# Performance work log

Hardware: AMD Instinct MI355X
Metric: run time of the kernel (lower is better)

The kernel has to match this reference:

```python
import jax, jax.numpy as jnp
import numpy as np

B, KD, VD = 65536, 512, 512

def setup_inputs() -> dict:
    key = jax.random.key(0)
    ks = jax.random.split(key, 5)
    return {
        "k": jax.random.normal(ks[0], (B, KD), jnp.float32),
        "v": jax.random.normal(ks[1], (B, VD), jnp.float32),
        "W": jax.random.normal(ks[2], (VD, KD), jnp.float32) * 0.02,  # memory.weight
        "S": jax.random.normal(ks[3], (VD, KD), jnp.float32) * 0.01,  # momentum buffer
        "gate_w": jax.random.normal(ks[4], (3, KD), jnp.float32) * 0.02,
        "gate_b": jnp.full((3,), 0.5, jnp.float32),  # nn.init.constant_(bias, 0.5)
    }

def reference(k, v, W, S, gate_w, gate_b):
    sg = jax.lax.stop_gradient
    # memory lookup: Linear(key_dim -> val_dim), no bias
    retrieved = k @ W.T                           # (B, VD)
    diff = retrieved - sg(v)
    loss_memory = jnp.mean(diff * diff)
    # --- TTT update (training path; all detached from autodiff in torch) ---
    # autograd.grad of mse(memory(k), v) w.r.t. W is analytically an outer product:
    # grad = 2/(B*VD) * (k @ W.T - v).T @ k
    d = sg(diff)                                  # loss_ttt uses detached k, v -> same residual values
    grad = (2.0 / (B * VD)) * (d.T @ sg(k))       # (VD, KD)
    # gates from batch-mean key
    gates = jax.nn.sigmoid(gate_w @ sg(jnp.mean(k, axis=0)) + gate_b)  # (3,)
    alpha, eta, theta = gates[0], gates[1], gates[2]
    new_S = eta * sg(S) - theta * grad            # momentum decay + gradient step
    new_W = (1.0 - alpha) * sg(W) + new_S         # gated weight decay + momentum write
    return retrieved, loss_memory, new_W, new_S
```

## Files before the change

kernel.cpp:

```cpp
#include <hip/hip_runtime.h>
#include <hip/hip_bf16.h>

typedef __attribute__((ext_vector_type(8))) short bf16x8;
typedef __attribute__((ext_vector_type(4))) float f32x4;
typedef unsigned int u32;
typedef unsigned short u16;

#define NB 65536
#define NKD 512
#define NVD 512

#define WS_COLSUM 262144
#define WS_LOSS   262656
#define WS_DIFFT_BYTES 1056768

#define OUT_LOSS 33554432
#define OUT_W    33554433
#define OUT_S    33816577

__device__ inline u32 pkbf2(float a, float b) {
    __hip_bfloat162 h2 = __float22bfloat162_rn(make_float2(a, b));
    u32 r;
    __builtin_memcpy(&r, &h2, 4);
    return r;
}

__device__ inline void async16(const u16* g, u16* l) {
    __builtin_amdgcn_global_load_lds(
        (const __attribute__((address_space(1))) u32*)g,
        (__attribute__((address_space(3))) u32*)l, 16, 0, 0);
}

#define PA 72
#define PT 136

__global__ __launch_bounds__(256, 2)
void k1_gemm1(const float* __restrict__ kmat, const float* __restrict__ vmat,
              const float* __restrict__ Wmat, float* __restrict__ out,
              float* __restrict__ ws, u16* __restrict__ diffT) {
    __shared__ u16 sm[18432];
    __shared__ float lred[4];

    const int tid = threadIdx.x;
    const int bx = blockIdx.x;
    const int rowtile = bx >> 2, ntile = bx & 3;
    const long b0 = (long)rowtile * 128;
    const int vd0 = ntile * 128;
    const int wv = tid >> 6, lane = tid & 63;
    const int wm = wv & 1, wn = wv >> 1;
    const int col = lane & 15, kg = lane >> 4;

    const int srow = tid >> 4;
    const int scol = (tid & 15) * 4;

    f32x4 acc[4][4] = {};

    for (int it = 0; it < 8; ++it) {
        __syncthreads();
        const float* gA = kmat + (b0 + srow) * 512 + it * 64 + scol;
        const float* gB = Wmat + (long)(vd0 + srow) * 512 + it * 64 + scol;
#pragma unroll
        for (int i = 0; i < 8; ++i) {
            float4 a = *(const float4*)(gA + (long)i * 16 * 512);
            float4 b = *(const float4*)(gB + (long)i * 16 * 512);
            int r = i * 16 + srow;
            *(uint2*)&sm[r * PA + scol] = make_uint2(pkbf2(a.x, a.y), pkbf2(a.z, a.w));
            *(uint2*)&sm[9216 + r * PA + scol] = make_uint2(pkbf2(b.x, b.y), pkbf2(b.z, b.w));
        }
        __syncthreads();
#pragma unroll
        for (int kk = 0; kk < 2; ++kk) {
            bf16x8 af[4], bfr[4];
#pragma unroll
            for (int i = 0; i < 4; ++i)
                af[i] = *(const bf16x8*)&sm[(wm * 64 + i * 16 + col) * PA + kk * 32 + kg * 8];
#pragma unroll
            for (int j = 0; j < 4; ++j)
                bfr[j] = *(const bf16x8*)&sm[9216 + (wn * 64 + j * 16 + col) * PA + kk * 32 + kg * 8];
#pragma unroll
            for (int i = 0; i < 4; ++i)
#pragma unroll
                for (int j = 0; j < 4; ++j)
                    acc[i][j] = __builtin_amdgcn_mfma_f32_16x16x32_bf16(af[i], bfr[j], acc[i][j], 0, 0, 0);
        }
    }

    __syncthreads();
    u16* smT = sm;

    float lossp = 0.f;
    const int rg = lane >> 4;
#pragma unroll
    for (int i = 0; i < 4; ++i) {
#pragma unroll
        for (int j = 0; j < 4; ++j) {
            int r0 = wm * 64 + i * 16 + rg * 4;
            int c  = wn * 64 + j * 16 + col;
            long gb = b0 + r0;
            float dd[4];
#pragma unroll
            for (int r = 0; r < 4; ++r) {
                float rv = acc[i][j][r];
                long gidx = (gb + r) * 512 + vd0 + c;
                out[gidx] = rv;
                float dv = rv - vmat[gidx];
                lossp += dv * dv;
                dd[r] = dv;
            }
            *(u32*)&smT[c * PT + r0]     = pkbf2(dd[0], dd[1]);
            *(u32*)&smT[c * PT + r0 + 2] = pkbf2(dd[2], dd[3]);
        }
    }

#pragma unroll
    for (int m = 32; m; m >>= 1) lossp += __shfl_xor(lossp, m);
    if (lane == 0) lred[wv] = lossp;
    __syncthreads();
    if (tid == 0) atomicAdd(&ws[WS_LOSS], lred[0] + lred[1] + lred[2] + lred[3]);

    {
        const int c = tid >> 1, h = tid & 1;
        const u16* src = &smT[c * PT + h * 64];
        u16* dst = diffT + ((long)(vd0 + c) << 16) + b0 + h * 64;
#pragma unroll
        for (int q = 0; q < 8; ++q) {
            uint4 t4 = *(const uint4*)(src + q * 8);
            *(uint4*)(dst + q * 8) = t4;
        }
    }
}

__global__ __launch_bounds__(256, 2)
void k2_grad(const u16* __restrict__ diffT, const float* __restrict__ kmat,
             float* __restrict__ ws) {
    __shared__ u16 sm[17408];
    u16* As = sm;
    u16* Bs = sm + 8192;

    const int tid = threadIdx.x;
    const int bx = blockIdx.x;
    const int tile = bx & 15, chunk = bx >> 4;
    const int vd0 = (tile >> 2) * 128, kd0 = (tile & 3) * 128;
    const long b0 = (long)chunk * 2048;
    const int wv = tid >> 6, lane = tid & 63;
    const int wm = wv & 1, wn = wv >> 1;
    const int col = lane & 15, kg = lane >> 4;

    const int bcol = (tid & 63) * 2;
    const int bq = wv * 16;

    f32x4 acc[4][4] = {};
    float cs0 = 0.f, cs1 = 0.f;

    for (int it = 0; it < 32; ++it) {
        __syncthreads();
        {
            const u16* gbase = diffT + ((long)vd0 << 16) + b0 + it * 64;
#pragma unroll
            for (int q = 0; q < 4; ++q) {
                int rowb = wv * 32 + q * 8;
                const u16* g = gbase + ((long)(rowb + (lane >> 3)) << 16) + (lane & 7) * 8;
                async16(g, &As[rowb * 64]);
            }
        }
        {
            const float* gk = kmat + (b0 + it * 64 + bq) * 512 + kd0 + bcol;
            float2 r[16];
#pragma unroll
            for (int i = 0; i < 16; ++i) r[i] = *(const float2*)(gk + (long)i * 512);
#pragma unroll
            for (int i = 0; i < 16; ++i) { cs0 += r[i].x; cs1 += r[i].y; }
            u32 p0[8], p1[8];
#pragma unroll
            for (int i = 0; i < 8; ++i) {
                p0[i] = pkbf2(r[2 * i].x, r[2 * i + 1].x);
                p1[i] = pkbf2(r[2 * i].y, r[2 * i + 1].y);
            }
            *(uint4*)&Bs[bcol * PA + bq]           = make_uint4(p0[0], p0[1], p0[2], p0[3]);
            *(uint4*)&Bs[bcol * PA + bq + 8]       = make_uint4(p0[4], p0[5], p0[6], p0[7]);
            *(uint4*)&Bs[(bcol + 1) * PA + bq]     = make_uint4(p1[0], p1[1], p1[2], p1[3]);
            *(uint4*)&Bs[(bcol + 1) * PA + bq + 8] = make_uint4(p1[4], p1[5], p1[6], p1[7]);
        }
        __syncthreads();
#pragma unroll
        for (int kk = 0; kk < 2; ++kk) {
            bf16x8 af[4], bfr[4];
#pragma unroll
            for (int i = 0; i < 4; ++i)
                af[i] = *(const bf16x8*)&As[(wm * 64 + i * 16 + col) * 64 + kk * 32 + kg * 8];
#pragma unroll
            for (int j = 0; j < 4; ++j)
                bfr[j] = *(const bf16x8*)&Bs[(wn * 64 + j * 16 + col) * PA + kk * 32 + kg * 8];
#pragma unroll
            for (int i = 0; i < 4; ++i)
#pragma unroll
                for (int j = 0; j < 4; ++j)
                    acc[i][j] = __builtin_amdgcn_mfma_f32_16x16x32_bf16(af[i], bfr[j], acc[i][j], 0, 0, 0);
        }
    }

    const int rg = lane >> 4;
#pragma unroll
    for (int i = 0; i < 4; ++i)
#pragma unroll
        for (int j = 0; j < 4; ++j)
#pragma unroll
            for (int r = 0; r < 4; ++r) {
                int vd = vd0 + wm * 64 + i * 16 + rg * 4 + r;
                int kd = kd0 + wn * 64 + j * 16 + col;
                atomicAdd(&ws[vd * 512 + kd], acc[i][j][r]);
            }

    if (vd0 == 0) {
        __syncthreads();
        float* cred = (float*)sm;
        cred[bcol * 4 + wv] = cs0;
        cred[(bcol + 1) * 4 + wv] = cs1;
        __syncthreads();
        if (tid < 128) {
            float s = cred[tid * 4] + cred[tid * 4 + 1] + cred[tid * 4 + 2] + cred[tid * 4 + 3];
            atomicAdd(&ws[WS_COLSUM + kd0 + tid], s);
        }
    }
}

__global__ __launch_bounds__(256)
void k3_final(const float* __restrict__ Wmat, const float* __restrict__ Smat,
              const float* __restrict__ gw, const float* __restrict__ gb,
              const float* __restrict__ ws, float* __restrict__ out) {
    __shared__ float gates[3];
    const int tid = threadIdx.x;
    if (tid < 64) {
        float d0 = 0.f, d1 = 0.f, d2 = 0.f;
#pragma unroll
        for (int i = 0; i < 8; ++i) {
            int kd = i * 64 + tid;
            float km = ws[WS_COLSUM + kd] * (1.0f / 65536.0f);
            d0 += gw[kd] * km;
            d1 += gw[512 + kd] * km;
            d2 += gw[1024 + kd] * km;
        }
#pragma unroll
        for (int m = 32; m; m >>= 1) {
            d0 += __shfl_xor(d0, m);
            d1 += __shfl_xor(d1, m);
            d2 += __shfl_xor(d2, m);
        }
        if (tid == 0) {
            gates[0] = 1.f / (1.f + __expf(-(d0 + gb[0])));
            gates[1] = 1.f / (1.f + __expf(-(d1 + gb[1])));
            gates[2] = 1.f / (1.f + __expf(-(d2 + gb[2])));
        }
    }
    __syncthreads();
    const float alpha = gates[0], eta = gates[1], theta = gates[2];
    const int i = blockIdx.x * 256 + tid;
    float g = ws[i] * 5.9604644775390625e-8f;
    float ns = eta * Smat[i] - theta * g;
    out[OUT_S + i] = ns;
    out[OUT_W + i] = (1.f - alpha) * Wmat[i] + ns;
    if (blockIdx.x == 0 && tid == 0)
        out[OUT_LOSS] = ws[WS_LOSS] * 2.98023223876953125e-8f;
}

extern "C" void kernel_launch(void* const* d_in, const int* in_sizes, int n_in,
                              void* d_out, int out_size, void* d_ws, size_t ws_size,
                              hipStream_t stream) {
    const float* k  = (const float*)d_in[0];
    const float* v  = (const float*)d_in[1];
    const float* W  = (const float*)d_in[2];
    const float* S  = (const float*)d_in[3];
    const float* gw = (const float*)d_in[4];
    const float* gb = (const float*)d_in[5];
    float* out = (float*)d_out;
    float* ws  = (float*)d_ws;
    u16* diffT = (u16*)((char*)d_ws + WS_DIFFT_BYTES);

    hipMemsetAsync(d_ws, 0, (WS_LOSS + 1) * sizeof(float), stream);

    hipLaunchKernelGGL(k1_gemm1, dim3(2048), dim3(256), 0, stream, k, v, W, out, ws, diffT);
    hipLaunchKernelGGL(k2_grad,  dim3(512),  dim3(256), 0, stream, diffT, k, ws);
    hipLaunchKernelGGL(k3_final, dim3(1024), dim3(256), 0, stream, W, S, gw, gb, ws, out);
}
```

Before: 566.8 us.

## Replace residual-based gradient with Gram-matrix formulation and trace-based loss

```diff
diff --git a/kernel.cpp b/kernel.cpp
--- a/kernel.cpp
+++ b/kernel.cpp
@@ -6,13 +6,14 @@
 typedef unsigned int u32;
 typedef unsigned short u16;
 
-#define NB 65536
-#define NKD 512
-#define NVD 512
-
-#define WS_COLSUM 262144
-#define WS_LOSS   262656
-#define WS_DIFFT_BYTES 1056768
+#define WS_G1     0
+#define WS_G2     262144
+#define WS_COLSUM 524288
+#define WS_VSQ    524800
+#define WS_GATES  524801
+#define WS_TR1    524804
+#define WS_TR2    524805
+#define WS_PART   524808
 
 #define OUT_LOSS 33554432
 #define OUT_W    33554433
@@ -25,177 +26,199 @@
     return r;
 }
 
-__device__ inline void async16(const u16* g, u16* l) {
-    __builtin_amdgcn_global_load_lds(
-        (const __attribute__((address_space(1))) u32*)g,
-        (__attribute__((address_space(3))) u32*)l, 16, 0, 0);
-}
-
-#define PA 72
-#define PT 136
-
-__global__ __launch_bounds__(256, 2)
-void k1_gemm1(const float* __restrict__ kmat, const float* __restrict__ vmat,
-              const float* __restrict__ Wmat, float* __restrict__ out,
-              float* __restrict__ ws, u16* __restrict__ diffT) {
+__device__ inline void jobdec(int j, int& isG2, int& rt, int& ct) {
+    if (j >= 10) { isG2 = 1; rt = (j - 10) >> 2; ct = (j - 10) & 3; }
+    else {
+        isG2 = 0;
+        if (j < 4)      { rt = 0; ct = j; }
+        else if (j < 7) { rt = 1; ct = j - 3; }
+        else if (j < 9) { rt = 2; ct = j - 5; }
+        else            { rt = 3; ct = 3; }
+    }
+}
+
+__global__ __launch_bounds__(256, 3)
+void kg_gram(const float* __restrict__ kmat, const float* __restrict__ vmat,
+             float* __restrict__ ws) {
     __shared__ u16 sm[18432];
-    __shared__ float lred[4];
+    u16* As = sm;
+    u16* Bs = sm + 9216;
 
     const int tid = threadIdx.x;
     const int bx = blockIdx.x;
-    const int rowtile = bx >> 2, ntile = bx & 3;
-    const long b0 = (long)rowtile * 128;
-    const int vd0 = ntile * 128;
+    const int c = bx & 31;
+    const int j = bx >> 5;
+    int isG2, rt, ct;
+    jobdec(j, isG2, rt, ct);
+    const float* Asrc = (isG2 ? vmat : kmat) + rt * 128;
+    const float* Bsrc = kmat + ct * 128;
+    const bool doCS = isG2 && (rt == 0);
+    const bool doVS = isG2 && (ct == 0);
+    const long b0 = (long)c * 2048;
+
     const int wv = tid >> 6, lane = tid & 63;
     const int wm = wv & 1, wn = wv >> 1;
     const int col = lane & 15, kg = lane >> 4;
-
-    const int srow = tid >> 4;
-    const int scol = (tid & 15) * 4;
+    const int bcol = (tid & 63) * 2;
+    const int bq = wv * 16;
 
     f32x4 acc[4][4] = {};
-
-    for (int it = 0; it < 8; ++it) {
-        __syncthreads();
-        const float* gA = kmat + (b0 + srow) * 512 + it * 64 + scol;
-        const float* gB = Wmat + (long)(vd0 + srow) * 512 + it * 64 + scol;
-#pragma unroll
-        for (int i = 0; i < 8; ++i) {
-            float4 a = *(const float4*)(gA + (long)i * 16 * 512);
-            float4 b = *(const float4*)(gB + (long)i * 16 * 512);
-            int r = i * 16 + srow;
-            *(uint2*)&sm[r * PA + scol] = make_uint2(pkbf2(a.x, a.y), pkbf2(a.z, a.w));
-            *(uint2*)&sm[9216 + r * PA + scol] = make_uint2(pkbf2(b.x, b.y), pkbf2(b.z, b.w));
-        }
-        __syncthreads();
+    float cs0 = 0.f, cs1 = 0.f, vs = 0.f;
+
+    float2 aR[16], bR[16];
+    {
+        const float* ga = Asrc + (b0 + bq) * 512 + bcol;
+        const float* gb = Bsrc + (b0 + bq) * 512 + bcol;
+#pragma unroll
+        for (int i = 0; i < 16; ++i) {
+            aR[i] = *(const float2*)(ga + (long)i * 512);
+            bR[i] = *(const float2*)(gb + (long)i * 512);
+        }
+    }
+
+    for (int it = 0; it < 32; ++it) {
+        __syncthreads();
+        if (doVS) {
+#pragma unroll
+            for (int i = 0; i < 16; ++i) vs += aR[i].x * aR[i].x + aR[i].y * aR[i].y;
+        }
+        if (doCS) {
+#pragma unroll
+            for (int i = 0; i < 16; ++i) { cs0 += bR[i].x; cs1 += bR[i].y; }
+        }
+        *(uint4*)&As[bcol * 72 + bq] = make_uint4(
+            pkbf2(aR[0].x, aR[1].x), pkbf2(aR[2].x, aR[3].x),
+            pkbf2(aR[4].x, aR[5].x), pkbf2(aR[6].x, aR[7].x));
+        *(uint4*)&As[bcol * 72 + bq + 8] = make_uint4(
+            pkbf2(aR[8].x, aR[9].x), pkbf2(aR[10].x, aR[11].x),
+            pkbf2(aR[12].x, aR[13].x), pkbf2(aR[14].x, aR[15].x));
+        *(uint4*)&As[(bcol + 1) * 72 + bq] = make_uint4(
+            pkbf2(aR[0].y, aR[1].y), pkbf2(aR[2].y, aR[3].y),
+            pkbf2(aR[4].y, aR[5].y), pkbf2(aR[6].y, aR[7].y));
+        *(uint4*)&As[(bcol + 1) * 72 + bq + 8] = make_uint4(
+            pkbf2(aR[8].y, aR[9].y), pkbf2(aR[10].y, aR[11].y),
+            pkbf2(aR[12].y, aR[13].y), pkbf2(aR[14].y, aR[15].y));
+        *(uint4*)&Bs[bcol * 72 + bq] = make_uint4(
+            pkbf2(bR[0].x, bR[1].x), pkbf2(bR[2].x, bR[3].x),
+            pkbf2(bR[4].x, bR[5].x), pkbf2(bR[6].x, bR[7].x));
+        *(uint4*)&Bs[bcol * 72 + bq + 8] = make_uint4(
+            pkbf2(bR[8].x, bR[9].x), pkbf2(bR[10].x, bR[11].x),
+            pkbf2(bR[12].x, bR[13].x), pkbf2(bR[14].x, bR[15].x));
+        *(uint4*)&Bs[(bcol + 1) * 72 + bq] = make_uint4(
+            pkbf2(bR[0].y, bR[1].y), pkbf2(bR[2].y, bR[3].y),
+            pkbf2(bR[4].y, bR[5].y), pkbf2(bR[6].y, bR[7].y));
+        *(uint4*)&Bs[(bcol + 1) * 72 + bq + 8] = make_uint4(
+            pkbf2(bR[8].y, bR[9].y), pkbf2(bR[10].y, bR[11].y),
+            pkbf2(bR[12].y, bR[13].y), pkbf2(bR[14].y, bR[15].y));
+        __syncthreads();
+        if (it < 31) {
+            const float* ga = Asrc + (b0 + (it + 1) * 64 + bq) * 512 + bcol;
+            const float* gb = Bsrc + (b0 + (it + 1) * 64 + bq) * 512 + bcol;
+#pragma unroll
+            for (int i = 0; i < 16; ++i) {
+                aR[i] = *(const float2*)(ga + (long)i * 512);
+                bR[i] = *(const float2*)(gb + (long)i * 512);
+            }
+        }
 #pragma unroll
         for (int kk = 0; kk < 2; ++kk) {
             bf16x8 af[4], bfr[4];
 #pragma unroll
             for (int i = 0; i < 4; ++i)
-                af[i] = *(const bf16x8*)&sm[(wm * 64 + i * 16 + col) * PA + kk * 32 + kg * 8];
-#pragma unroll
-            for (int j = 0; j < 4; ++j)
-                bfr[j] = *(const bf16x8*)&sm[9216 + (wn * 64 + j * 16 + col) * PA + kk * 32 + kg * 8];
+                af[i] = *(const bf16x8*)&As[(wm * 64 + i * 16 + col) * 72 + kk * 32 + kg * 8];
+#pragma unroll
+            for (int jj = 0; jj < 4; ++jj)
+                bfr[jj] = *(const bf16x8*)&Bs[(wn * 64 + jj * 16 + col) * 72 + kk * 32 + kg * 8];
 #pragma unroll
             for (int i = 0; i < 4; ++i)
 #pragma unroll
-                for (int j = 0; j < 4; ++j)
-                    acc[i][j] = __builtin_amdgcn_mfma_f32_16x16x32_bf16(af[i], bfr[j], acc[i][j], 0, 0, 0);
-        }
-    }
-
-    __syncthreads();
-    u16* smT = sm;
-
-    float lossp = 0.f;
-    const int rg = lane >> 4;
-#pragma unroll
-    for (int i = 0; i < 4; ++i) {
-#pragma unroll
-        for (int j = 0; j < 4; ++j) {
-            int r0 = wm * 64 + i * 16 + rg * 4;
-            int c  = wn * 64 + j * 16 + col;
-            long gb = b0 + r0;
-            float dd[4];
-#pragma unroll
-            for (int r = 0; r < 4; ++r) {
-                float rv = acc[i][j][r];
-                long gidx = (gb + r) * 512 + vd0 + c;
-                out[gidx] = rv;
-                float dv = rv - vmat[gidx];
-                lossp += dv * dv;
-                dd[r] = dv;
-            }
-            *(u32*)&smT[c * PT + r0]     = pkbf2(dd[0], dd[1]);
-            *(u32*)&smT[c * PT + r0 + 2] = pkbf2(dd[2], dd[3]);
-        }
-    }
-
-#pragma unroll
-    for (int m = 32; m; m >>= 1) lossp += __shfl_xor(lossp, m);
-    if (lane == 0) lred[wv] = lossp;
-    __syncthreads();
-    if (tid == 0) atomicAdd(&ws[WS_LOSS], lred[0] + lred[1] + lred[2] + lred[3]);
-
-    {
-        const int c = tid >> 1, h = tid & 1;
-        const u16* src = &smT[c * PT + h * 64];
-        u16* dst = diffT + ((long)(vd0 + c) << 16) + b0 + h * 64;
-#pragma unroll
-        for (int q = 0; q < 8; ++q) {
-            uint4 t4 = *(const uint4*)(src + q * 8);
-            *(uint4*)(dst + q * 8) = t4;
-        }
-    }
-}
-
-__global__ __launch_bounds__(256, 2)
-void k2_grad(const u16* __restrict__ diffT, const float* __restrict__ kmat,
-             float* __restrict__ ws) {
-    __shared__ u16 sm[17408];
-    u16* As = sm;
-    u16* Bs = sm + 8192;
-
+                for (int jj = 0; jj < 4; ++jj)
+                    acc[i][jj] = __builtin_amdgcn_mfma_f32_16x16x32_bf16(af[i], bfr[jj], acc[i][jj], 0, 0, 0);
+        }
+    }
+
+    float* pout = ws + WS_PART + ((long)(j * 32 + c) * 256 + tid) * 64;
+#pragma unroll
+    for (int i = 0; i < 4; ++i)
+#pragma unroll
+        for (int jj = 0; jj < 4; ++jj)
+            *(f32x4*)(pout + (i * 4 + jj) * 4) = acc[i][jj];
+
+    if (doVS) {
+#pragma unroll
+        for (int m = 32; m; m >>= 1) vs += __shfl_xor(vs, m);
+        if (lane == 0) atomicAdd(&ws[WS_VSQ], vs);
+    }
+    if (doCS) {
+        __syncthreads();
+        float* cred = (float*)sm;
+        cred[bcol * 4 + wv] = cs0;
+        cred[(bcol + 1) * 4 + wv] = cs1;
+        __syncthreads();
+        if (tid < 128) {
+            float s = cred[tid * 4] + cred[tid * 4 + 1] + cred[tid * 4 + 2] + cred[tid * 4 + 3];
+            atomicAdd(&ws[WS_COLSUM + ct * 128 + tid], s);
+        }
+    }
+}
+
+__global__ __launch_bounds__(256, 3)
+void k1_retr(const float* __restrict__ kmat, const float* __restrict__ Wmat,
+             float* __restrict__ out) {
+    __shared__ u16 sm[18432];
     const int tid = threadIdx.x;
     const int bx = blockIdx.x;
-    const int tile = bx & 15, chunk = bx >> 4;
-    const int vd0 = (tile >> 2) * 128, kd0 = (tile & 3) * 128;
-    const long b0 = (long)chunk * 2048;
+    const int rowtile = bx & 511, nt = bx >> 9;
+    const long b0 = (long)rowtile * 128;
+    const int vd0 = nt * 128;
     const int wv = tid >> 6, lane = tid & 63;
     const int wm = wv & 1, wn = wv >> 1;
     const int col = lane & 15, kg = lane >> 4;
-
-    const int bcol = (tid & 63) * 2;
-    const int bq = wv * 16;
+    const int srow = tid >> 4, scol = (tid & 15) * 4;
 
     f32x4 acc[4][4] = {};
-    float cs0 = 0.f, cs1 = 0.f;
-
-    for (int it = 0; it < 32; ++it) {
-        __syncthreads();
-        {
-            const u16* gbase = diffT + ((long)vd0 << 16) + b0 + it * 64;
-#pragma unroll
-            for (int q = 0; q < 4; ++q) {
-                int rowb = wv * 32 + q * 8;
-                const u16* g = gbase + ((long)(rowb + (lane >> 3)) << 16) + (lane & 7) * 8;
-                async16(g, &As[rowb * 64]);
+    const float* gA0 = kmat + (b0 + srow) * 512 + scol;
+    const float* gB0 = Wmat + (long)(vd0 + srow) * 512 + scol;
+
+    float4 aR[8], bR[8];
+#pragma unroll
+    for (int i = 0; i < 8; ++i) {
+        aR[i] = *(const float4*)(gA0 + (long)i * 16 * 512);
+        bR[i] = *(const float4*)(gB0 + (long)i * 16 * 512);
+    }
+
+    for (int it = 0; it < 8; ++it) {
+        __syncthreads();
+#pragma unroll
+        for (int i = 0; i < 8; ++i) {
+            int r = i * 16 + srow;
+            *(uint2*)&sm[r * 72 + scol] = make_uint2(pkbf2(aR[i].x, aR[i].y), pkbf2(aR[i].z, aR[i].w));
+            *(uint2*)&sm[9216 + r * 72 + scol] = make_uint2(pkbf2(bR[i].x, bR[i].y), pkbf2(bR[i].z, bR[i].w));
+        }
+        __syncthreads();
+        if (it < 7) {
+            const float* ga = gA0 + (it + 1) * 64;
+            const float* gb = gB0 + (it + 1) * 64;
+#pragma unroll
+            for (int i = 0; i < 8; ++i) {
+                aR[i] = *(const float4*)(ga + (long)i * 16 * 512);
+                bR[i] = *(const float4*)(gb + (long)i * 16 * 512);
             }
         }
-        {
-            const float* gk = kmat + (b0 + it * 64 + bq) * 512 + kd0 + bcol;
-            float2 r[16];
-#pragma unroll
-            for (int i = 0; i < 16; ++i) r[i] = *(const float2*)(gk + (long)i * 512);
-#pragma unroll
-            for (int i = 0; i < 16; ++i) { cs0 += r[i].x; cs1 += r[i].y; }
-            u32 p0[8], p1[8];
-#pragma unroll
-            for (int i = 0; i < 8; ++i) {
-                p0[i] = pkbf2(r[2 * i].x, r[2 * i + 1].x);
-                p1[i] = pkbf2(r[2 * i].y, r[2 * i + 1].y);
-            }
-            *(uint4*)&Bs[bcol * PA + bq]           = make_uint4(p0[0], p0[1], p0[2], p0[3]);
-            *(uint4*)&Bs[bcol * PA + bq + 8]       = make_uint4(p0[4], p0[5], p0[6], p0[7]);
-            *(uint4*)&Bs[(bcol + 1) * PA + bq]     = make_uint4(p1[0], p1[1], p1[2], p1[3]);
-            *(uint4*)&Bs[(bcol + 1) * PA + bq + 8] = make_uint4(p1[4], p1[5], p1[6], p1[7]);
-        }
-        __syncthreads();
 #pragma unroll
         for (int kk = 0; kk < 2; ++kk) {
             bf16x8 af[4], bfr[4];
 #pragma unroll
             for (int i = 0; i < 4; ++i)
-                af[i] = *(const bf16x8*)&As[(wm * 64 + i * 16 + col) * 64 + kk * 32 + kg * 8];
-#pragma unroll
-            for (int j = 0; j < 4; ++j)
-                bfr[j] = *(const bf16x8*)&Bs[(wn * 64 + j * 16 + col) * PA + kk * 32 + kg * 8];
+                af[i] = *(const bf16x8*)&sm[(wm * 64 + i * 16 + col) * 72 + kk * 32 + kg * 8];
+#pragma unroll
+            for (int jj = 0; jj < 4; ++jj)
+                bfr[jj] = *(const bf16x8*)&sm[9216 + (wn * 64 + jj * 16 + col) * 72 + kk * 32 + kg * 8];
 #pragma unroll
             for (int i = 0; i < 4; ++i)
 #pragma unroll
-                for (int j = 0; j < 4; ++j)
-                    acc[i][j] = __builtin_amdgcn_mfma_f32_16x16x32_bf16(af[i], bfr[j], acc[i][j], 0, 0, 0);
+                for (int jj = 0; jj < 4; ++jj)
+                    acc[i][jj] = __builtin_amdgcn_mfma_f32_16x16x32_bf16(af[i], bfr[jj], acc[i][jj], 0, 0, 0);
         }
     }
 
@@ -203,38 +226,59 @@
 #pragma unroll
     for (int i = 0; i < 4; ++i)
 #pragma unroll
-        for (int j = 0; j < 4; ++j)
-#pragma unroll
-            for (int r = 0; r < 4; ++r) {
-                int vd = vd0 + wm * 64 + i * 16 + rg * 4 + r;
-                int kd = kd0 + wn * 64 + j * 16 + col;
-                atomicAdd(&ws[vd * 512 + kd], acc[i][j][r]);
-            }
-
-    if (vd0 == 0) {
-        __syncthreads();
-        float* cred = (float*)sm;
-        cred[bcol * 4 + wv] = cs0;
-        cred[(bcol + 1) * 4 + wv] = cs1;
-        __syncthreads();
-        if (tid < 128) {
-            float s = cred[tid * 4] + cred[tid * 4 + 1] + cred[tid * 4 + 2] + cred[tid * 4 + 3];
-            atomicAdd(&ws[WS_COLSUM + kd0 + tid], s);
-        }
-    }
+        for (int jj = 0; jj < 4; ++jj) {
+            int r0 = wm * 64 + i * 16 + rg * 4;
+            int cc = wn * 64 + jj * 16 + col;
+            long gb = b0 + r0;
+#pragma unroll
+            for (int r = 0; r < 4; ++r)
+                out[(gb + r) * 512 + vd0 + cc] = acc[i][jj][r];
+        }
 }
 
 __global__ __launch_bounds__(256)
-void k3_final(const float* __restrict__ Wmat, const float* __restrict__ Smat,
-              const float* __restrict__ gw, const float* __restrict__ gb,
-              const float* __restrict__ ws, float* __restrict__ out) {
-    __shared__ float gates[3];
-    const int tid = threadIdx.x;
-    if (tid < 64) {
+void k2_reduce(float* __restrict__ ws, const float* __restrict__ gw,
+               const float* __restrict__ gb) {
+    const int g = blockIdx.x * 256 + threadIdx.x;
+    const int j = g >> 12;
+    const int s = g & 4095;
+    const int tp = s >> 4;
+    const int grp = s & 15;
+
+    f32x4 sum = {};
+    const float* pbase = ws + WS_PART + ((long)j * 8192 + tp) * 64 + grp * 4;
+#pragma unroll 8
+    for (int c = 0; c < 32; ++c)
+        sum += *(const f32x4*)(pbase + (long)c * 16384);
+
+    const int wm = (tp >> 6) & 1, wn = tp >> 7;
+    const int l = tp & 63, rg = l >> 4, cl = l & 15;
+    const int i = grp >> 2, jj = grp & 3;
+    const int m0 = wm * 64 + i * 16 + rg * 4;
+    const int n = wn * 64 + jj * 16 + cl;
+
+    int isG2, rt, ct;
+    jobdec(j, isG2, rt, ct);
+    const int r0 = rt * 128, c0 = ct * 128;
+    if (!isG2) {
+#pragma unroll
+        for (int q = 0; q < 4; ++q) {
+            float val = sum[q];
+            ws[WS_G1 + (r0 + m0 + q) * 512 + c0 + n] = val;
+            if (rt != ct) ws[WS_G1 + (c0 + n) * 512 + r0 + m0 + q] = val;
+        }
+    } else {
+#pragma unroll
+        for (int q = 0; q < 4; ++q)
+            ws[WS_G2 + (r0 + m0 + q) * 512 + c0 + n] = sum[q];
+    }
+
+    if (blockIdx.x == 0 && threadIdx.x < 64) {
+        const int t = threadIdx.x;
         float d0 = 0.f, d1 = 0.f, d2 = 0.f;
 #pragma unroll
-        for (int i = 0; i < 8; ++i) {
-            int kd = i * 64 + tid;
+        for (int ii = 0; ii < 8; ++ii) {
+            int kd = ii * 64 + t;
             float km = ws[WS_COLSUM + kd] * (1.0f / 65536.0f);
             d0 += gw[kd] * km;
             d1 += gw[512 + kd] * km;
@@ -246,21 +290,62 @@
             d1 += __shfl_xor(d1, m);
             d2 += __shfl_xor(d2, m);
         }
-        if (tid == 0) {
-            gates[0] = 1.f / (1.f + __expf(-(d0 + gb[0])));
-            gates[1] = 1.f / (1.f + __expf(-(d1 + gb[1])));
-            gates[2] = 1.f / (1.f + __expf(-(d2 + gb[2])));
-        }
-    }
-    __syncthreads();
-    const float alpha = gates[0], eta = gates[1], theta = gates[2];
-    const int i = blockIdx.x * 256 + tid;
-    float g = ws[i] * 5.9604644775390625e-8f;
-    float ns = eta * Smat[i] - theta * g;
-    out[OUT_S + i] = ns;
-    out[OUT_W + i] = (1.f - alpha) * Wmat[i] + ns;
-    if (blockIdx.x == 0 && tid == 0)
-        out[OUT_LOSS] = ws[WS_LOSS] * 2.98023223876953125e-8f;
+        if (t == 0) {
+            ws[WS_GATES + 0] = 1.f / (1.f + __expf(-(d0 + gb[0])));
+            ws[WS_GATES + 1] = 1.f / (1.f + __expf(-(d1 + gb[1])));
+            ws[WS_GATES + 2] = 1.f / (1.f + __expf(-(d2 + gb[2])));
+        }
+    }
+}
+
+__global__ __launch_bounds__(256)
+void k3_main(const float* __restrict__ Wmat, const float* __restrict__ Smat,
+             float* __restrict__ ws, float* __restrict__ out) {
+    const int g = blockIdx.x * 256 + threadIdx.x;
+    const int m = g >> 7;
+    const int n0 = (g & 127) * 4;
+    const float* wrow = Wmat + m * 512;
+
+    f32x4 acc = {};
+    for (int jx = 0; jx < 512; jx += 4) {
+#pragma unroll
+        for (int t = 0; t < 4; ++t) {
+            float wsc = wrow[jx + t];
+            f32x4 g1 = *(const f32x4*)(ws + WS_G1 + (jx + t) * 512 + n0);
+            acc += g1 * wsc;
+        }
+    }
+    f32x4 g2 = *(const f32x4*)(ws + WS_G2 + m * 512 + n0);
+    f32x4 w4 = *(const f32x4*)(Wmat + m * 512 + n0);
+    f32x4 s4 = *(const f32x4*)(Smat + m * 512 + n0);
+    const float alpha = ws[WS_GATES], eta = ws[WS_GATES + 1], theta = ws[WS_GATES + 2];
+    const float c1 = 5.9604644775390625e-8f;
+
+    f32x4 grad = (acc - g2) * c1;
+    f32x4 ns = s4 * eta - grad * theta;
+    f32x4 nw = w4 * (1.f - alpha) + ns;
+    const int base = m * 512 + n0;
+#pragma unroll
+    for (int q = 0; q < 4; ++q) {
+        out[OUT_S + base + q] = ns[q];
+        out[OUT_W + base + q] = nw[q];
+    }
+
+    float t1 = acc[0] * w4[0] + acc[1] * w4[1] + acc[2] * w4[2] + acc[3] * w4[3];
+    float t2 = g2[0] * w4[0] + g2[1] * w4[1] + g2[2] * w4[2] + g2[3] * w4[3];
+#pragma unroll
+    for (int mm = 32; mm; mm >>= 1) {
+        t1 += __shfl_xor(t1, mm);
+        t2 += __shfl_xor(t2, mm);
+    }
+    if ((threadIdx.x & 63) == 0) {
+        atomicAdd(&ws[WS_TR1], t1);
+        atomicAdd(&ws[WS_TR2], t2);
+    }
+}
+
+__global__ void k3_loss(const float* __restrict__ ws, float* __restrict__ out) {
+    out[OUT_LOSS] = (ws[WS_TR1] - 2.f * ws[WS_TR2] + ws[WS_VSQ]) * 2.98023223876953125e-8f;
 }
 
 extern "C" void kernel_launch(void* const* d_in, const int* in_sizes, int n_in,
@@ -274,11 +359,12 @@
     const float* gb = (const float*)d_in[5];
     float* out = (float*)d_out;
     float* ws  = (float*)d_ws;
-    u16* diffT = (u16*)((char*)d_ws + WS_DIFFT_BYTES);
-
-    hipMemsetAsync(d_ws, 0, (WS_LOSS + 1) * sizeof(float), stream);
-
-    hipLaunchKernelGGL(k1_gemm1, dim3(2048), dim3(256), 0, stream, k, v, W, out, ws, diffT);
-    hipLaunchKernelGGL(k2_grad,  dim3(512),  dim3(256), 0, stream, diffT, k, ws);
-    hipLaunchKernelGGL(k3_final, dim3(1024), dim3(256), 0, stream, W, S, gw, gb, ws, out);
-}
+
+    hipMemsetAsync((char*)d_ws + (size_t)WS_COLSUM * 4, 0, 518 * 4, stream);
+
+    hipLaunchKernelGGL(kg_gram,   dim3(832),  dim3(256), 0, stream, k, v, ws);
+    hipLaunchKernelGGL(k1_retr,   dim3(2048), dim3(256), 0, stream, k, W, out);
+    hipLaunchKernelGGL(k2_reduce, dim3(416),  dim3(256), 0, stream, ws, gw, gb);
+    hipLaunchKernelGGL(k3_main,   dim3(256),  dim3(256), 0, stream, W, S, ws, out);
+    hipLaunchKernelGGL(k3_loss,   dim3(1),    dim3(1),   0, stream, ws, out);
+}
```

After: 623.2 us. 10.0% more time.
